# Optimization experiments

Hardware: AMD Instinct MI355X
Metric: run time of the kernel (lower is better)

Reference implementation:

```python
import jax, jax.numpy as jnp
import numpy as np

D_MODEL = 768
NUM_HEADS = 12
HEAD_DIM = D_MODEL // NUM_HEADS
D_FF = 3072
LN_EPS = 1e-5


def _xavier(key, shape):
    # nn.init.xavier_uniform_ on a [out, in] Linear weight
    fan_out, fan_in = shape[-2], shape[-1]
    limit = float(np.sqrt(6.0 / (fan_in + fan_out)))
    return jax.random.uniform(key, shape, jnp.float32, -limit, limit)


def setup_inputs() -> dict:
    key = jax.random.key(0)
    ks = jax.random.split(key, 10)
    x = jax.random.normal(ks[0], (4, 2048, D_MODEL), jnp.float32)
    # per-head projections stacked: [H, head_dim, d_model] (torch Linear weight layout [out, in])
    Wq = _xavier(ks[1], (NUM_HEADS, HEAD_DIM, D_MODEL))
    Wk = _xavier(ks[2], (NUM_HEADS, HEAD_DIM, D_MODEL))
    Wv = _xavier(ks[3], (NUM_HEADS, HEAD_DIM, D_MODEL))
    Wo = _xavier(ks[4], (D_MODEL, D_MODEL))
    W1 = jax.random.normal(ks[5], (D_FF, D_MODEL), jnp.float32) * 0.02
    b1 = jnp.zeros((D_FF,), jnp.float32)
    W2 = jax.random.normal(ks[6], (D_MODEL, D_FF), jnp.float32) * 0.02
    b2 = jnp.zeros((D_MODEL,), jnp.float32)
    g1 = jnp.ones((D_MODEL,), jnp.float32)
    be1 = jnp.zeros((D_MODEL,), jnp.float32)
    g2 = jnp.ones((D_MODEL,), jnp.float32)
    be2 = jnp.zeros((D_MODEL,), jnp.float32)
    return {"x": x, "Wq": Wq, "Wk": Wk, "Wv": Wv, "Wo": Wo,
            "W1": W1, "b1": b1, "W2": W2, "b2": b2,
            "g1": g1, "be1": be1, "g2": g2, "be2": be2}


def _layernorm(x, g, b):
    mu = jnp.mean(x, axis=-1, keepdims=True)
    var = jnp.mean(jnp.square(x - mu), axis=-1, keepdims=True)
    return (x - mu) * jax.lax.rsqrt(var + LN_EPS) * g + b


def reference(x, Wq, Wk, Wv, Wo, W1, b1, W2, b2, g1, be1, g2, be2):
    B, S, D = x.shape
    # all heads batched (same math as the per-head Python loop + concat)
    q = jnp.einsum('bsd,hed->bhse', x, Wq)   # [B,H,S,e]
    k = jnp.einsum('bsd,hed->bhse', x, Wk)
    v = jnp.einsum('bsd,hed->bhse', x, Wv)
    scores = jnp.einsum('bhse,bhte->bhst', q, k) / jnp.sqrt(jnp.float32(HEAD_DIM))
    attn = jax.nn.softmax(scores, axis=-1)
    ctx = jnp.einsum('bhst,bhte->bhse', attn, v)
    # concat heads along feature dim (head order matches stacking order)
    concat = ctx.transpose(0, 2, 1, 3).reshape(B, S, D)
    attn_out = concat @ Wo.T
    h = _layernorm(x + attn_out, g1, be1)
    ffn = jax.nn.relu(h @ W1.T + b1) @ W2.T + b2
    out = _layernorm(h + ffn, g2, be2)
    return out
```

## Files before the change

kernel.cpp:

```cpp
#include <hip/hip_runtime.h>

typedef unsigned short u16;
typedef unsigned int u32;
typedef __attribute__((ext_vector_type(8))) short short8;
typedef __attribute__((ext_vector_type(4))) float f32x4;
typedef __attribute__((ext_vector_type(4))) unsigned short u16x4;

extern "C" __device__ float __ocml_native_exp2_f32(float);
#define EXP2(x) __ocml_native_exp2_f32(x)

__device__ __forceinline__ float b2f(u16 u){
  union { float f; unsigned int i; } c; c.i = ((unsigned int)u) << 16; return c.f;
}
__device__ __forceinline__ u16 f2b(float f){
  union { float f; unsigned int i; } c; c.f = f;
  unsigned int i = c.i;
  unsigned int r = (i + 0x7FFFu + ((i >> 16) & 1u)) >> 16;
  return (u16)r;
}

#define GLD16(gp, lp) __builtin_amdgcn_global_load_lds( \
    (const __attribute__((address_space(1))) void*)(gp), \
    (__attribute__((address_space(3))) void*)(lp), 16, 0, 0)

__device__ __forceinline__ u32 pkbf(float lo, float hi){
  u32 r;
  asm volatile("v_cvt_pk_bf16_f32 %0, %1, %2" : "=v"(r) : "v"(lo), "v"(hi));
  return r;
}

__global__ __launch_bounds__(256) void cvt_all(
    const float* __restrict__ s0, const float* __restrict__ s1,
    const float* __restrict__ s2, const float* __restrict__ s3,
    const float* __restrict__ s4, const float* __restrict__ s5,
    const float* __restrict__ s6, u16* __restrict__ dst)
{
  const int i = (blockIdx.x * 256 + threadIdx.x) * 4;
  const float* sp;
  if      (i <  6291456) sp = s0 + i;
  else if (i <  6881280) sp = s1 + (i - 6291456);
  else if (i <  7471104) sp = s2 + (i - 6881280);
  else if (i <  8060928) sp = s3 + (i - 7471104);
  else if (i <  8650752) sp = s4 + (i - 8060928);
  else if (i < 11010048) sp = s5 + (i - 8650752);
  else                   sp = s6 + (i - 11010048);
  float4 f = *(const float4*)sp;
  u16x4 o = { f2b(f.x), f2b(f.y), f2b(f.z), f2b(f.w) };
  *(u16x4*)(dst + i) = o;
}

enum { EPI_QKV = 0, EPI_WO = 1, EPI_FFN1 = 2, EPI_FFN2 = 3 };
__device__ __forceinline__ float KSCALE_C(){ return 0.125f * 1.44269504088896340736f; }

template<int EPI>
__global__ __launch_bounds__(256) void gemm_bt(
    const u16* __restrict__ A, const u16* __restrict__ Bm,
    int K, int gx,
    u16* __restrict__ outB,
    const float* __restrict__ auxF,
    const u16* __restrict__ auxB)
{
  __shared__ __align__(16) short Asm[128][32];
  __shared__ __align__(16) short Bsm[128][32];
  const int tid  = threadIdx.x;
  const int lane = tid & 63;
  const int wid  = tid >> 6;
  const int wr = wid >> 1, wc = wid & 1;
  const int fr = lane & 15, fq = lane >> 4;

  const int nwg = gridDim.x;
  const int lin = blockIdx.x;
  const int wg  = (lin & 7) * (nwg >> 3) + (lin >> 3);
  const int bx = wg % gx, by = wg / gx;
  const int m0 = by * 128, n0 = bx * 128;

  f32x4 acc[4][4];
#pragma unroll
  for (int i = 0; i < 4; i++)
#pragma unroll
    for (int j = 0; j < 4; j++) acc[i][j] = (f32x4){0.f, 0.f, 0.f, 0.f};

  const int lrow = lane >> 2;
  const int lcol = (lane & 3) << 3;

  for (int k0 = 0; k0 < K; k0 += 32) {
    const u16* ga = A  + (size_t)(m0 + wid*32 + lrow) * K + k0 + lcol;
    const u16* gb = Bm + (size_t)(n0 + wid*32 + lrow) * K + k0 + lcol;
    GLD16(ga,                 &Asm[wid*32][0]);
    GLD16(ga + (size_t)16*K,  &Asm[wid*32 + 16][0]);
    GLD16(gb,                 &Bsm[wid*32][0]);
    GLD16(gb + (size_t)16*K,  &Bsm[wid*32 + 16][0]);
    __syncthreads();

    short8 a[4], b[4];
#pragma unroll
    for (int i = 0; i < 4; i++) a[i] = *(const short8*)&Asm[wr*64 + i*16 + fr][fq*8];
#pragma unroll
    for (int j = 0; j < 4; j++) b[j] = *(const short8*)&Bsm[wc*64 + j*16 + fr][fq*8];
    __builtin_amdgcn_s_setprio(1);
#pragma unroll
    for (int i = 0; i < 4; i++)
#pragma unroll
      for (int j = 0; j < 4; j++)
        acc[i][j] = __builtin_amdgcn_mfma_f32_16x16x32_bf16(a[i], b[j], acc[i][j], 0, 0, 0);
    __builtin_amdgcn_s_setprio(0);
    __syncthreads();
  }

#pragma unroll
  for (int i = 0; i < 4; i++) {
    const int row0 = m0 + wr*64 + i*16 + fq*4;
#pragma unroll
    for (int j = 0; j < 4; j++) {
      const int col = n0 + wc*64 + j*16 + fr;
#pragma unroll
      for (int r = 0; r < 4; r++) {
        const int row = row0 + r;
        float val = acc[i][j][r];
        if (EPI == EPI_QKV) {
          int tt = (col >= 1536) ? 2 : (col >= 768 ? 1 : 0);
          int rem = col - tt * 768;
          int h = rem >> 6, e = rem & 63;
          int bb = row >> 11, s = row & 2047;
          if (tt == 2) {
            size_t idx = (((size_t)(bb*12 + h)) * 64 + e) * 2048 + s;
            ((u16*)auxB)[idx] = f2b(val);
          } else {
            size_t idx = (((size_t)(tt*48 + bb*12 + h)) * 2048 + s) * 64 + e;
            if (tt == 1) val *= KSCALE_C();
            outB[idx] = f2b(val);
          }
        } else {
          float o = val + auxF[col];
          o = o > 0.f ? o : 0.f;
          outB[(size_t)row * 3072 + col] = f2b(o);
        }
      }
    }
  }
}

template<int EPI>
__global__ __launch_bounds__(256) void gemm_n64(
    const u16* __restrict__ A, const u16* __restrict__ Bm,
    int K,
    u16* __restrict__ outB,
    const float* __restrict__ auxF,
    const u16* __restrict__ auxB)
{
  __shared__ __align__(16) short Asm[128][32];
  __shared__ __align__(16) short Bsm[64][32];
  const int tid  = threadIdx.x;
  const int lane = tid & 63;
  const int wid  = tid >> 6;
  const int wr = wid >> 1, wc = wid & 1;
  const int fr = lane & 15, fq = lane >> 4;

  const int nwg = gridDim.x;
  const int lin = blockIdx.x;
  const int wg  = (lin & 7) * (nwg >> 3) + (lin >> 3);
  const int bx = wg % 12, by = wg / 12;
  const int m0 = by * 128, n0 = bx * 64;

  f32x4 acc[4][2];
#pragma unroll
  for (int i = 0; i < 4; i++)
#pragma unroll
    for (int j = 0; j < 2; j++) acc[i][j] = (f32x4){0.f, 0.f, 0.f, 0.f};

  const int lrow = lane >> 2;
  const int lcol = (lane & 3) << 3;

  for (int k0 = 0; k0 < K; k0 += 32) {
    const u16* ga = A  + (size_t)(m0 + wid*32 + lrow) * K + k0 + lcol;
    const u16* gb = Bm + (size_t)(n0 + wid*16 + lrow) * K + k0 + lcol;
    GLD16(ga,                 &Asm[wid*32][0]);
    GLD16(ga + (size_t)16*K,  &Asm[wid*32 + 16][0]);
    GLD16(gb,                 &Bsm[wid*16][0]);
    __syncthreads();

    short8 a[4], b[2];
#pragma unroll
    for (int i = 0; i < 4; i++) a[i] = *(const short8*)&Asm[wr*64 + i*16 + fr][fq*8];
#pragma unroll
    for (int j = 0; j < 2; j++) b[j] = *(const short8*)&Bsm[wc*32 + j*16 + fr][fq*8];
    __builtin_amdgcn_s_setprio(1);
#pragma unroll
    for (int i = 0; i < 4; i++)
#pragma unroll
      for (int j = 0; j < 2; j++)
        acc[i][j] = __builtin_amdgcn_mfma_f32_16x16x32_bf16(a[i], b[j], acc[i][j], 0, 0, 0);
    __builtin_amdgcn_s_setprio(0);
    __syncthreads();
  }

#pragma unroll
  for (int i = 0; i < 4; i++) {
    const int row0 = m0 + wr*64 + i*16 + fq*4;
#pragma unroll
    for (int j = 0; j < 2; j++) {
      const int col = n0 + wc*32 + j*16 + fr;
#pragma unroll
      for (int r = 0; r < 4; r++) {
        const int row = row0 + r;
        float val = acc[i][j][r];
        size_t idx = (size_t)row * 768 + col;
        if (EPI == EPI_WO) {
          outB[idx] = f2b(val + b2f(auxB[idx]));
        } else {
          outB[idx] = f2b(val + auxF[col] + b2f(auxB[idx]));
        }
      }
    }
  }
}

__global__ __launch_bounds__(512) void flash_attn(
    const u16* __restrict__ q, const u16* __restrict__ kmat, const u16* __restrict__ vtmat,
    u16* __restrict__ ctx)
{
  const int tid = threadIdx.x;
  const int lane = tid & 63, wid = tid >> 6;
  const int fr = lane & 15, fq = lane >> 4;
  const int orig = blockIdx.x;
  const int wg = (orig & 7) * 96 + (orig >> 3);
  const int qb = wg & 15;
  const int ph = wg >> 4;
  const size_t plane = (size_t)ph * 2048 * 64;
  const u16* qp  = q + plane;
  const u16* kp  = kmat + plane;
  const u16* vtp = vtmat + plane;

  __shared__ __align__(16) short Ksm[2][64][64];
  __shared__ __align__(16) short Vsm[2][64][64];

  const int qr0 = qb*128 + wid*16;
  const short8 aq0 = *(const short8*)(qp + (size_t)(qr0 + fr)*64 + fq*8);
  const short8 aq1 = *(const short8*)(qp + (size_t)(qr0 + fr)*64 + 32 + fq*8);

  short8 vones;
#pragma unroll
  for (int j = 0; j < 8; j++) vones[j] = (short)0x3F80;

  const int rA = wid*8 + (lane >> 3);
  const int cA = (((lane & 7) ^ ((rA & 3) | (((rA >> 3) & 1) << 2)))) * 8;

#define STAGE(B, KT) do { \
    GLD16(kp  + (size_t)((KT)*64 + rA)*64 + cA,  &Ksm[B][wid*8][0]); \
    GLD16(vtp + (size_t)rA*2048 + (KT)*64 + cA,  &Vsm[B][wid*8][0]); \
  } while(0)

  f32x4 o[4];
#pragma unroll
  for (int eb = 0; eb < 4; eb++) o[eb] = (f32x4){0.f, 0.f, 0.f, 0.f};
  float m = -1e30f, l = 0.f;
  const f32x4 zero = (f32x4){0.f, 0.f, 0.f, 0.f};

  STAGE(0, 0);
  __syncthreads();

  const int fK  = (fr & 3) | (((fr >> 2) & 1) << 2);
  const int kc0 = ((fq    ) ^ fK) * 8;
  const int kc1 = ((4 + fq) ^ fK) * 8;
  const int krow = (fr & 3) + 8 * (fr >> 2);
  const int fV  = (fr & 3) | (((fr >> 3) & 1) << 2);
  const int vc0 = ((fq    ) ^ fV) * 8;
  const int vc1 = ((4 + fq) ^ fV) * 8;

  int buf = 0;
  for (int kt = 0; kt < 32; ++kt) {
    if (kt < 31) STAGE(buf ^ 1, kt + 1);

    f32x4 st[2][2];
    __builtin_amdgcn_s_setprio(1);
#pragma unroll
    for (int h = 0; h < 2; h++)
#pragma unroll
      for (int c = 0; c < 2; c++) {
        const short* kr = &Ksm[buf][32*h + 4*c + krow][0];
        short8 kf0 = *(const short8*)(kr + kc0);
        short8 kf1 = *(const short8*)(kr + kc1);
        f32x4 a = __builtin_amdgcn_mfma_f32_16x16x32_bf16(kf0, aq0, zero, 0, 0, 0);
        st[h][c]  = __builtin_amdgcn_mfma_f32_16x16x32_bf16(kf1, aq1, a,    0, 0, 0);
      }
    __builtin_amdgcn_s_setprio(0);

    float t0 = fmaxf(fmaxf(st[0][0][0], st[0][0][1]), st[0][0][2]);
    float t1 = fmaxf(fmaxf(st[0][0][3], st[0][1][0]), st[0][1][1]);
    float t2 = fmaxf(fmaxf(st[0][1][2], st[0][1][3]), st[1][0][0]);
    float t3 = fmaxf(fmaxf(st[1][0][1], st[1][0][2]), st[1][0][3]);
    float t4 = fmaxf(fmaxf(st[1][1][0], st[1][1][1]), st[1][1][2]);
    float u0 = fmaxf(fmaxf(t0, t1), st[1][1][3]);
    float u1 = fmaxf(fmaxf(t2, t3), t4);
    float lm = fmaxf(u0, u1);
    lm = fmaxf(lm, __shfl_xor(lm, 16));
    lm = fmaxf(lm, __shfl_xor(lm, 32));

    if (!__all(lm <= m + 8.f)) {
      float nm = fmaxf(m, lm);
      float corr = EXP2(m - nm);
      m = nm;
      l *= corr;
#pragma unroll
      for (int eb = 0; eb < 4; eb++)
#pragma unroll
        for (int r = 0; r < 4; r++) o[eb][r] *= corr;
    }

    float p[2][2][4];
#pragma unroll
    for (int h = 0; h < 2; h++)
#pragma unroll
      for (int c = 0; c < 2; c++)
#pragma unroll
        for (int r = 0; r < 4; r++)
          p[h][c][r] = EXP2(st[h][c][r] - m);

    union { u32 u[4]; short8 s8; } pf0, pf1;
    pf0.u[0] = pkbf(p[0][0][0], p[0][0][1]);
    pf0.u[1] = pkbf(p[0][0][2], p[0][0][3]);
    pf0.u[2] = pkbf(p[0][1][0], p[0][1][1]);
    pf0.u[3] = pkbf(p[0][1][2], p[0][1][3]);
    pf1.u[0] = pkbf(p[1][0][0], p[1][0][1]);
    pf1.u[1] = pkbf(p[1][0][2], p[1][0][3]);
    pf1.u[2] = pkbf(p[1][1][0], p[1][1][1]);
    pf1.u[3] = pkbf(p[1][1][2], p[1][1][3]);

    __builtin_amdgcn_s_setprio(1);
    f32x4 ol = __builtin_amdgcn_mfma_f32_16x16x32_bf16(vones, pf0.s8, zero, 0, 0, 0);
    ol       = __builtin_amdgcn_mfma_f32_16x16x32_bf16(vones, pf1.s8, ol,   0, 0, 0);
#pragma unroll
    for (int eb = 0; eb < 4; eb++) {
      const short* vr = &Vsm[buf][eb*16 + fr][0];
      o[eb] = __builtin_amdgcn_mfma_f32_16x16x32_bf16(*(const short8*)(vr + vc0), pf0.s8, o[eb], 0, 0, 0);
      o[eb] = __builtin_amdgcn_mfma_f32_16x16x32_bf16(*(const short8*)(vr + vc1), pf1.s8, o[eb], 0, 0, 0);
    }
    __builtin_amdgcn_s_setprio(0);
    l += ol[0];

    __syncthreads();
    buf ^= 1;
  }
#undef STAGE

  const float inv = 1.0f / l;
  const int s = qr0 + fr;
  u16* cp = ctx + ((size_t)((ph/12)*2048 + s)) * 768 + (ph%12)*64;
#pragma unroll
  for (int eb = 0; eb < 4; eb++) {
    u16x4 w = { f2b(o[eb][0]*inv), f2b(o[eb][1]*inv), f2b(o[eb][2]*inv), f2b(o[eb][3]*inv) };
    *(u16x4*)(cp + eb*16 + fq*4) = w;
  }
}

template<int F32OUT>
__global__ __launch_bounds__(256) void ln_k(const u16* __restrict__ in,
    const float* __restrict__ g, const float* __restrict__ be, void* __restrict__ outp)
{
  const int lane = threadIdx.x & 63, wid = threadIdx.x >> 6;
  const int row = blockIdx.x * 4 + wid;
  const u16* p = in + (size_t)row * 768;
  float v[12];
  float s = 0.f, s2 = 0.f;
#pragma unroll
  for (int i = 0; i < 6; i++) {
    ushort2 uv = *(const ushort2*)(p + i*128 + lane*2);
    v[2*i]   = b2f(uv.x);
    v[2*i+1] = b2f(uv.y);
    s += v[2*i] + v[2*i+1];
    s2 += v[2*i]*v[2*i] + v[2*i+1]*v[2*i+1];
  }
#pragma unroll
  for (int msk = 1; msk < 64; msk <<= 1) { s += __shfl_xor(s, msk); s2 += __shfl_xor(s2, msk); }
  const float mu = s * (1.f/768.f);
  const float var = s2 * (1.f/768.f) - mu*mu;
  const float rstd = rsqrtf(var + 1e-5f);
#pragma unroll
  for (int i = 0; i < 6; i++) {
    int c = i*128 + lane*2;
    float o0 = (v[2*i]   - mu) * rstd * g[c]   + be[c];
    float o1 = (v[2*i+1] - mu) * rstd * g[c+1] + be[c+1];
    if (F32OUT) {
      float2 w = { o0, o1 };
      *(float2*)((float*)outp + (size_t)row*768 + c) = w;
    } else {
      ushort2 w = { f2b(o0), f2b(o1) };
      *(ushort2*)((u16*)outp + (size_t)row*768 + c) = w;
    }
  }
}

extern "C" void kernel_launch(void* const* d_in, const int* in_sizes, int n_in,
                              void* d_out, int out_size, void* d_ws, size_t ws_size,
                              hipStream_t stream)
{
  const float* x   = (const float*)d_in[0];
  const float* Wq  = (const float*)d_in[1];
  const float* Wk  = (const float*)d_in[2];
  const float* Wv  = (const float*)d_in[3];
  const float* Wo  = (const float*)d_in[4];
  const float* W1  = (const float*)d_in[5];
  const float* b1  = (const float*)d_in[6];
  const float* W2  = (const float*)d_in[7];
  const float* b2  = (const float*)d_in[8];
  const float* g1  = (const float*)d_in[9];
  const float* be1 = (const float*)d_in[10];
  const float* g2  = (const float*)d_in[11];
  const float* be2 = (const float*)d_in[12];
  float* out = (float*)d_out;

  char* ws = (char*)d_ws;
  u16* xb     = (u16*)(ws + 0);
  u16* Wqkv_b = (u16*)(ws + 12582912);
  u16* Wo_b   = (u16*)(ws + 16121856);
  u16* W1_b   = (u16*)(ws + 17301504);
  u16* W2_b   = (u16*)(ws + 22020096);
  u16* qkv    = (u16*)(ws + 26738688);
  u16* ctxb   = (u16*)(ws + 64487424);
  u16* hidden = (u16*)(ws + 26738688);
  u16* vt     = (u16*)(ws + 77070336);
  u16* resid1 = (u16*)(ws + 77070336);
  u16* hb     = (u16*)(ws + 102236160);
  u16* pre2   = (u16*)(ws + 77070336);

  cvt_all<<<dim3(13056), 256, 0, stream>>>(x, Wq, Wk, Wv, Wo, W1, W2, (u16*)ws);

  gemm_bt<EPI_QKV><<<dim3(1152), 256, 0, stream>>>(
      xb, Wqkv_b, 768, 18, qkv, nullptr, vt);

  u16* qb_ = qkv;
  u16* kb_ = qkv + 6291456;

  flash_attn<<<dim3(768), 512, 0, stream>>>(qb_, kb_, vt, ctxb);

  gemm_n64<EPI_WO><<<dim3(768), 256, 0, stream>>>(
      ctxb, Wo_b, 768, resid1, nullptr, xb);

  ln_k<0><<<2048, 256, 0, stream>>>(resid1, g1, be1, hb);

  gemm_bt<EPI_FFN1><<<dim3(1536), 256, 0, stream>>>(
      hb, W1_b, 768, 24, hidden, b1, nullptr);

  gemm_n64<EPI_FFN2><<<dim3(768), 256, 0, stream>>>(
      hidden, W2_b, 3072, pre2, b2, hb);

  ln_k<1><<<2048, 256, 0, stream>>>(pre2, g2, be2, out);
}
```

Before: 306.0 us.

## Double-buffer LDS tiles and XOR-swizzle columns in GEMM kernels

Both GEMM kernels now use two LDS buffers and prefetch the next K tile via global_load_lds while computing on the current one. This removes one barrier per iteration and overlaps memory with MFMA work. The LDS column chunks are also XOR-swizzled by row, on both the global load side and the fragment read side, to reduce bank conflicts. LDS usage doubles, which may lower occupancy.

```diff
diff --git a/kernel.cpp b/kernel.cpp
--- a/kernel.cpp
+++ b/kernel.cpp
@@ -60,8 +60,8 @@
     const float* __restrict__ auxF,
     const u16* __restrict__ auxB)
 {
-  __shared__ __align__(16) short Asm[128][32];
-  __shared__ __align__(16) short Bsm[128][32];
+  __shared__ __align__(16) short Asm[2][128][32];
+  __shared__ __align__(16) short Bsm[2][128][32];
   const int tid  = threadIdx.x;
   const int lane = tid & 63;
   const int wid  = tid >> 6;
@@ -81,22 +81,30 @@
     for (int j = 0; j < 4; j++) acc[i][j] = (f32x4){0.f, 0.f, 0.f, 0.f};
 
   const int lrow = lane >> 2;
-  const int lcol = (lane & 3) << 3;
-
-  for (int k0 = 0; k0 < K; k0 += 32) {
-    const u16* ga = A  + (size_t)(m0 + wid*32 + lrow) * K + k0 + lcol;
-    const u16* gb = Bm + (size_t)(n0 + wid*32 + lrow) * K + k0 + lcol;
-    GLD16(ga,                 &Asm[wid*32][0]);
-    GLD16(ga + (size_t)16*K,  &Asm[wid*32 + 16][0]);
-    GLD16(gb,                 &Bsm[wid*32][0]);
-    GLD16(gb + (size_t)16*K,  &Bsm[wid*32 + 16][0]);
-    __syncthreads();
-
+  const int sc   = (((lane & 3) ^ ((lrow >> 1) & 3))) << 3;
+  const int rc   = ((fq ^ ((fr >> 1) & 3))) << 3;
+
+#define GSTAGE(b, kt) do { \
+    const u16* ga_ = A  + (size_t)(m0 + wid*32 + lrow) * K + (kt)*32 + sc; \
+    const u16* gb_ = Bm + (size_t)(n0 + wid*32 + lrow) * K + (kt)*32 + sc; \
+    GLD16(ga_,                 &Asm[b][wid*32][0]); \
+    GLD16(ga_ + (size_t)16*K,  &Asm[b][wid*32 + 16][0]); \
+    GLD16(gb_,                 &Bsm[b][wid*32][0]); \
+    GLD16(gb_ + (size_t)16*K,  &Bsm[b][wid*32 + 16][0]); \
+  } while(0)
+
+  const int NT = K >> 5;
+  GSTAGE(0, 0);
+  __syncthreads();
+
+  int bufn = 0;
+  for (int kt = 0; kt < NT; ++kt) {
+    if (kt + 1 < NT) GSTAGE(bufn ^ 1, kt + 1);
     short8 a[4], b[4];
 #pragma unroll
-    for (int i = 0; i < 4; i++) a[i] = *(const short8*)&Asm[wr*64 + i*16 + fr][fq*8];
-#pragma unroll
-    for (int j = 0; j < 4; j++) b[j] = *(const short8*)&Bsm[wc*64 + j*16 + fr][fq*8];
+    for (int i = 0; i < 4; i++) a[i] = *(const short8*)&Asm[bufn][wr*64 + i*16 + fr][rc];
+#pragma unroll
+    for (int j = 0; j < 4; j++) b[j] = *(const short8*)&Bsm[bufn][wc*64 + j*16 + fr][rc];
     __builtin_amdgcn_s_setprio(1);
 #pragma unroll
     for (int i = 0; i < 4; i++)
@@ -105,7 +113,9 @@
         acc[i][j] = __builtin_amdgcn_mfma_f32_16x16x32_bf16(a[i], b[j], acc[i][j], 0, 0, 0);
     __builtin_amdgcn_s_setprio(0);
     __syncthreads();
-  }
+    bufn ^= 1;
+  }
+#undef GSTAGE
 
 #pragma unroll
   for (int i = 0; i < 4; i++) {
@@ -148,8 +158,8 @@
     const float* __restrict__ auxF,
     const u16* __restrict__ auxB)
 {
-  __shared__ __align__(16) short Asm[128][32];
-  __shared__ __align__(16) short Bsm[64][32];
+  __shared__ __align__(16) short Asm[2][128][32];
+  __shared__ __align__(16) short Bsm[2][64][32];
   const int tid  = threadIdx.x;
   const int lane = tid & 63;
   const int wid  = tid >> 6;
@@ -169,21 +179,29 @@
     for (int j = 0; j < 2; j++) acc[i][j] = (f32x4){0.f, 0.f, 0.f, 0.f};
 
   const int lrow = lane >> 2;
-  const int lcol = (lane & 3) << 3;
-
-  for (int k0 = 0; k0 < K; k0 += 32) {
-    const u16* ga = A  + (size_t)(m0 + wid*32 + lrow) * K + k0 + lcol;
-    const u16* gb = Bm + (size_t)(n0 + wid*16 + lrow) * K + k0 + lcol;
-    GLD16(ga,                 &Asm[wid*32][0]);
-    GLD16(ga + (size_t)16*K,  &Asm[wid*32 + 16][0]);
-    GLD16(gb,                 &Bsm[wid*16][0]);
-    __syncthreads();
-
+  const int sc   = (((lane & 3) ^ ((lrow >> 1) & 3))) << 3;
+  const int rc   = ((fq ^ ((fr >> 1) & 3))) << 3;
+
+#define GSTAGE(b, kt) do { \
+    const u16* ga_ = A  + (size_t)(m0 + wid*32 + lrow) * K + (kt)*32 + sc; \
+    const u16* gb_ = Bm + (size_t)(n0 + wid*16 + lrow) * K + (kt)*32 + sc; \
+    GLD16(ga_,                 &Asm[b][wid*32][0]); \
+    GLD16(ga_ + (size_t)16*K,  &Asm[b][wid*32 + 16][0]); \
+    GLD16(gb_,                 &Bsm[b][wid*16][0]); \
+  } while(0)
+
+  const int NT = K >> 5;
+  GSTAGE(0, 0);
+  __syncthreads();
+
+  int bufn = 0;
+  for (int kt = 0; kt < NT; ++kt) {
+    if (kt + 1 < NT) GSTAGE(bufn ^ 1, kt + 1);
     short8 a[4], b[2];
 #pragma unroll
-    for (int i = 0; i < 4; i++) a[i] = *(const short8*)&Asm[wr*64 + i*16 + fr][fq*8];
-#pragma unroll
-    for (int j = 0; j < 2; j++) b[j] = *(const short8*)&Bsm[wc*32 + j*16 + fr][fq*8];
+    for (int i = 0; i < 4; i++) a[i] = *(const short8*)&Asm[bufn][wr*64 + i*16 + fr][rc];
+#pragma unroll
+    for (int j = 0; j < 2; j++) b[j] = *(const short8*)&Bsm[bufn][wc*32 + j*16 + fr][rc];
     __builtin_amdgcn_s_setprio(1);
 #pragma unroll
     for (int i = 0; i < 4; i++)
@@ -192,7 +210,9 @@
         acc[i][j] = __builtin_amdgcn_mfma_f32_16x16x32_bf16(a[i], b[j], acc[i][j], 0, 0, 0);
     __builtin_amdgcn_s_setprio(0);
     __syncthreads();
-  }
+    bufn ^= 1;
+  }
+#undef GSTAGE
 
 #pragma unroll
   for (int i = 0; i < 4; i++) {
```

After: 302.6 us. No clear change (-1.1%).
